# Kernel optimization log

Hardware: AMD Instinct MI355X
Metric: run time of the kernel (lower is better)

## Reference

```python
import jax, jax.numpy as jnp
import numpy as np

B, N, A = 2, 4096, 5
TOPK = 30
K_RBF = 16
MAX_AA = 22
MAXREL = 32
EDGE_IN = 16 + K_RBF * 25 + 14 + 16  # 446
EDGE_FEAT = 128
PI = 3.1415926


def l2norm(v, eps=1e-12):
    n = jnp.sqrt(jnp.sum(v * v, axis=-1, keepdims=True))
    return v / jnp.maximum(n, eps)


def gather_nodes(nodes, idx):
    # nodes: (B,N,C), idx: (B,N,K) -> (B,N,K,C)
    b, n, k = idx.shape
    flat = idx.reshape(b, n * k, 1)
    out = jnp.take_along_axis(nodes, flat, axis=1)
    return out.reshape(b, n, k, nodes.shape[-1])


def quaternions(R):
    # R: (...,3,3) -> unit quaternion (...,4)
    Rxx, Ryy, Rzz = R[..., 0, 0], R[..., 1, 1], R[..., 2, 2]
    mag = 0.5 * jnp.sqrt(jnp.abs(1.0 + jnp.stack([Rxx - Ryy - Rzz, -Rxx + Ryy - Rzz, -Rxx - Ryy + Rzz], -1)) + 1e-12)
    signs = jnp.sign(jnp.stack([R[..., 2, 1] - R[..., 1, 2], R[..., 0, 2] - R[..., 2, 0], R[..., 1, 0] - R[..., 0, 1]], -1))
    xyz = signs * mag
    w = jnp.sqrt(jax.nn.relu(1.0 + Rxx + Ryy + Rzz) + 1e-12)[..., None] / 2.0
    return l2norm(jnp.concatenate([xyz, w], -1))


def setup_inputs():
    key = jax.random.key(0)
    ks = jax.random.split(key, 12)
    X = jax.random.normal(ks[0], (B, N, A, 3), jnp.float32) * 3.0
    mask = jnp.ones((B, N), jnp.float32)
    mask_atoms = jnp.ones((B, N, A), jnp.float32)
    means = jax.random.normal(ks[1], (K_RBF,), jnp.float32)
    stds = jax.random.normal(ks[2], (K_RBF,), jnp.float32)
    mul_w = jax.random.normal(ks[3], (A * A,), jnp.float32)
    bias_w = jax.random.normal(ks[4], (A * A,), jnp.float32)
    aa_pair_embed = jax.random.normal(ks[5], (MAX_AA * MAX_AA, K_RBF), jnp.float32) * 0.02
    aa_pair_embed = aa_pair_embed.at[441].set(0.0)  # padding_idx
    relpos_embed = jax.random.normal(ks[6], (2 * MAXREL + 1, 16), jnp.float32) * 0.02
    mask_embed = jax.random.normal(ks[7], (2, 16), jnp.float32) * 0.02
    W1 = jax.random.normal(ks[8], (EDGE_IN, EDGE_IN), jnp.float32) / np.sqrt(EDGE_IN)
    b1 = jnp.zeros((EDGE_IN,), jnp.float32)
    W2 = jax.random.normal(ks[9], (EDGE_IN, EDGE_FEAT), jnp.float32) / np.sqrt(EDGE_IN)
    b2 = jnp.zeros((EDGE_FEAT,), jnp.float32)
    aa = jax.random.randint(ks[10], (B, N), 0, 21, jnp.int32)
    residue_idx = jnp.tile(jnp.arange(N, dtype=jnp.int32)[None, :], (B, 1))
    chain_labels = jax.random.randint(ks[11], (B, N), 0, 2, jnp.int32)
    return dict(X=X, mask=mask, mask_atoms=mask_atoms, means=means, stds=stds, mul_w=mul_w,
                bias_w=bias_w, aa_pair_embed=aa_pair_embed, relpos_embed=relpos_embed,
                mask_embed=mask_embed, W1=W1, b1=b1, W2=W2, b2=b2, aa=aa,
                residue_idx=residue_idx, chain_labels=chain_labels)


def reference(X, mask, mask_atoms, means, stds, mul_w, bias_w, aa_pair_embed, relpos_embed,
              mask_embed, W1, b1, W2, b2, aa, residue_idx, chain_labels):
    Ca = X[:, :, 1]  # (B,N,3) C-alpha
    # ---- _dist: spatial kNN over C-alpha ----
    mask2d = mask[:, :, None] * mask[:, None, :]
    dx = Ca[:, None, :, :] - Ca[:, :, None, :]
    D = mask2d * jnp.sqrt(jnp.sum(dx * dx, -1) + 1e-6)
    D_adj = D + (1.0 - mask2d) * jnp.max(D, -1, keepdims=True)
    _, E_idx = jax.lax.top_k(-D_adj, TOPK)  # smallest distances
    mask_attend = jnp.take_along_axis(mask2d, E_idx, axis=2)  # (B,N,K)
    # ---- orientation features (local frames + quaternions) ----
    ones3 = jnp.ones((B, 1, 3), X.dtype)
    u = l2norm(jnp.concatenate([ones3, Ca[:, 1:] - Ca[:, :-1]], 1))
    b_ = l2norm(jnp.concatenate([u[:, :-1] - u[:, 1:], ones3], 1))
    n_ = l2norm(jnp.concatenate([jnp.cross(u[:, :-1], u[:, 1:]), ones3], 1))
    lf = jnp.stack([b_, n_, jnp.cross(b_, n_)], axis=2)  # (B,N,3,3)
    X_nb = gather_nodes(Ca, E_idx)                       # (B,N,K,3)
    O_nb = gather_nodes(lf.reshape(B, N, 9), E_idx).reshape(B, N, TOPK, 3, 3)
    t = X_nb - Ca[:, :, None, :]
    t = jnp.einsum('bnij,bnkj->bnki', lf, t)
    t = l2norm(t) * mask_attend[..., None]
    r = jnp.einsum('bnji,bnkjl->bnkil', lf, O_nb)  # lf^T @ O_nb
    q = quaternions(r) * mask_attend[..., None]
    O_feat = jnp.concatenate([t, q, 1.0 - 2.0 * jnp.abs(t), 1.0 - 2.0 * jnp.abs(q)], -1)  # (B,N,K,14)
    # ---- positional / chain embeddings ----
    offset = residue_idx[:, :, None] - residue_idx[:, None, :]
    offset_nb = jnp.take_along_axis(offset, E_idx, 2)
    d_chain = (chain_labels[:, :, None] == chain_labels[:, None, :]).astype(jnp.int32)
    E_chains = jnp.take_along_axis(d_chain, E_idx, 2)
    d = jnp.clip(offset_nb + MAXREL, 0, 2 * MAXREL)
    E_pos = relpos_embed[d] + mask_embed[E_chains]  # (B,N,K,16)
    # ---- GaussianLayer: aa-pair embed + atom-pair distance RBF ----
    aa_pair = aa[:, :, None] * MAX_AA + aa[:, None, :]
    aa_nb = jnp.take_along_axis(aa_pair, E_idx, 2)
    feat_aapair = aa_pair_embed[aa_nb] * mask_attend[..., None]  # (B,N,K,16)
    nbX = gather_nodes(X.reshape(B, N, A * 3), E_idx).reshape(B, N, TOPK, A, 3)
    delta = nbX[:, :, :, :, None, :] - X[:, :, None, None, :, :]  # (B,N,K,A,A,3)
    Dab = jnp.sqrt(jnp.sum(delta * delta, -1) + 1e-12)            # (B,N,K,A,A)
    et = jnp.arange(A * A).reshape(A, A)
    xg = mul_w[et] * Dab + bias_w[et]
    m_nb = gather_nodes(mask_atoms, E_idx)  # (B,N,K,A)
    xg = xg * (m_nb[..., None, :] * m_nb[..., :, None])
    std = jnp.abs(stds) + 0.01
    g = jnp.exp(-0.5 * ((xg[..., None] - means) / std) ** 2) / ((2.0 * PI) ** 0.5 * std)
    gbf = g.reshape(B, N, TOPK, A * A * K_RBF) * mask_attend[..., None]  # (B,N,K,400)
    # ---- fuse and project (NonLinear gbf_proj) ----
    E = jnp.concatenate([E_pos, gbf, O_feat, feat_aapair], -1)  # (B,N,K,446)
    h = jax.nn.gelu(E @ W1 + b1, approximate=False)
    return h @ W2 + b2  # (B,N,K,128)
```

## Files before the change

kernel.cpp:

```cpp
#include <hip/hip_runtime.h>
#include <cstdint>
#include <cstddef>

#define NN 4096
#define TOPK_ 30
#define BN_TOT 8192
#define M_TOT 245760
#define KP 448
#define HSTRIDE 136
#define EF 128

typedef unsigned short u16;
typedef unsigned int u32;
typedef __attribute__((ext_vector_type(8))) short bf16x8;
typedef __attribute__((ext_vector_type(4))) float f32x4;

__device__ __forceinline__ float b2f(u16 u){ return __uint_as_float(((u32)u)<<16); }
__device__ __forceinline__ u16 f2b(float f){
  u32 u = __float_as_uint(f);
  return (u16)((u + 0x7FFFu + ((u>>16)&1u)) >> 16);
}
__device__ __forceinline__ float ldf(const void* p, long i, int fl){
  return fl ? ((const float*)p)[i] : b2f(((const u16*)p)[i]);
}
__device__ __forceinline__ int is_f32_flag(const u16* mask){
  return (((const u32*)mask)[0] == 0x3F800000u) ? 1 : 0;
}
__device__ __forceinline__ void norm3(float x,float y,float z,float&ox,float&oy,float&oz){
  float n = sqrtf(x*x+y*y+z*z); n = fmaxf(n, 1e-12f);
  ox=x/n; oy=y/n; oz=z/n;
}
__device__ __forceinline__ float sgn(float x){ return x>0.f?1.f:(x<0.f?-1.f:0.f); }
__device__ __forceinline__ float gelu_fast(float x){
  float y = 0.70710678118654752440f * x;
  float s = fabsf(y);
  float t = __builtin_amdgcn_rcpf(fmaf(0.3275911f, s, 1.0f));
  float p = fmaf(fmaf(fmaf(fmaf(1.061405429f, t, -1.453152027f), t, 1.421413741f), t,
                 -0.284496736f), t, 0.254829592f);
  float e = __expf(-y*y);
  float erfs = fmaf(-p*t, e, 1.0f);
  float erfy = (x >= 0.f) ? erfs : -erfs;
  float hx = 0.5f*x;
  return fmaf(hx, erfy, hx);
}
__device__ __forceinline__ u32 pk_bf16(float lo, float hi){
  u32 r;
  asm("v_cvt_pk_bf16_f32 %0, %1, %2" : "=v"(r) : "v"(lo), "v"(hi));
  return r;
}

__global__ __launch_bounds__(256) void prep_kernel(
    const void* __restrict__ X, const u16* __restrict__ mask,
    const void* __restrict__ W1, const void* __restrict__ b1,
    const void* __restrict__ W2, const void* __restrict__ b2,
    float* __restrict__ ca, float* __restrict__ lf,
    u16* __restrict__ W1P, u16* __restrict__ W2P,
    float* __restrict__ b1p, float* __restrict__ b2p)
{
  const int fl = is_f32_flag(mask);
  int idx = blockIdx.x*256 + threadIdx.x;
  if (idx < BN_TOT) {
    int i = idx & (NN-1);
    float cax = ldf(X, (long)idx*15+3, fl), cay = ldf(X, (long)idx*15+4, fl), caz = ldf(X, (long)idx*15+5, fl);
    ca[idx*4+0]=cax; ca[idx*4+1]=cay; ca[idx*4+2]=caz; ca[idx*4+3]=0.f;
    float bx,by,bz,nx,ny,nz;
    if (i < NN-1) {
      float uix,uiy,uiz;
      if (i==0) { norm3(1.f,1.f,1.f,uix,uiy,uiz); }
      else {
        float px=ldf(X,(long)(idx-1)*15+3,fl), py=ldf(X,(long)(idx-1)*15+4,fl), pz=ldf(X,(long)(idx-1)*15+5,fl);
        norm3(cax-px, cay-py, caz-pz, uix,uiy,uiz);
      }
      float qx=ldf(X,(long)(idx+1)*15+3,fl), qy=ldf(X,(long)(idx+1)*15+4,fl), qz=ldf(X,(long)(idx+1)*15+5,fl);
      float vx,vy,vz; norm3(qx-cax, qy-cay, qz-caz, vx,vy,vz);
      norm3(uix-vx, uiy-vy, uiz-vz, bx,by,bz);
      norm3(uiy*vz-uiz*vy, uiz*vx-uix*vz, uix*vy-uiy*vx, nx,ny,nz);
    } else {
      norm3(1.f,1.f,1.f,bx,by,bz); nx=bx; ny=by; nz=bz;
    }
    float cx = by*nz - bz*ny, cy = bz*nx - bx*nz, cz = bx*ny - by*nx;
    float* L = lf + (size_t)idx*12;
    L[0]=bx;L[1]=by;L[2]=bz;L[3]=nx;L[4]=ny;L[5]=nz;L[6]=cx;L[7]=cy;L[8]=cz;
    return;
  }
  int r1 = idx - BN_TOT;
  if (r1 < 229376) {
    int f = r1 >> 9, li = r1 & 511;
    int n0 = f / 14, kc = f - n0*14;
    int ln = li >> 3, j = li & 7;
    int n = n0*16 + (ln & 15);
    int k = kc*32 + (ln >> 4)*8 + j;
    W1P[r1] = (n < 446 && k < 446) ? (fl ? f2b(((const float*)W1)[(long)k*446 + n])
                                         : ((const u16*)W1)[(long)k*446 + n]) : (u16)0;
    return;
  }
  int r2 = r1 - 229376;
  if (r2 < 65536) {
    int f = r2 >> 9, li = r2 & 511;
    int n0 = f >> 4, kc = f & 15;
    int ln = li >> 3, j = li & 7;
    int n = n0*16 + (ln & 15);
    int k = kc*32 + (ln >> 4)*8 + j;
    W2P[r2] = (k < 446) ? (fl ? f2b(((const float*)W2)[(long)k*128 + n])
                              : ((const u16*)W2)[(long)k*128 + n]) : (u16)0;
    return;
  }
  int r3 = r2 - 65536;
  if (r3 < 512) { b1p[r3] = (r3<446)? ldf(b1, r3, fl) : 0.f; return; }
  int r4 = r3 - 512;
  if (r4 < 128) { b2p[r4] = ldf(b2, r4, fl); }
}

__global__ __launch_bounds__(64) void knn_kernel(const float4* __restrict__ ca,
                                                 int* __restrict__ eidx)
{
#pragma clang fp contract(off)
  __shared__ u32 keys[NN];
  int bi = blockIdx.x;
  int lane = threadIdx.x;
  int b = bi >> 12;
  const float4 ci = ca[bi];
  const float4* cab = ca + (b<<12);
  u32 mind = 0xFFFFFFFFu; int minj = 1<<30;
  for (int c = 0; c < 64; ++c) {
    int j = (c<<6) | lane;
    float4 cj = cab[j];
    float dx = cj.x-ci.x, dy = cj.y-ci.y, dz = cj.z-ci.z;
    float ss = dx*dx;
    ss = ss + dy*dy;
    ss = ss + dz*dz;
    float d = sqrtf(ss + 1e-6f);
    u32 db = __float_as_uint(d);
    keys[(c<<6)|lane] = db;
    if (db < mind) { mind = db; minj = j; }
  }
  __syncthreads();
  for (int r = 0; r < TOPK_; ++r) {
    u32 wd = mind; int wj = minj;
    #pragma unroll
    for (int off = 32; off; off >>= 1) {
      u32 od = __shfl_xor(wd, off, 64);
      int oj = __shfl_xor(wj, off, 64);
      if (od < wd || (od == wd && oj < wj)) { wd = od; wj = oj; }
    }
    if (lane == 0) eidx[bi*TOPK_ + r] = wj;
    int wl = wj & 63;
    if (lane == wl) keys[wj] = 0xFFFFFFFFu;
    __syncthreads();
    u32 kv = keys[(lane<<6)|wl];
    int kj = (lane<<6)|wl;
    #pragma unroll
    for (int off = 32; off; off >>= 1) {
      u32 od = __shfl_xor(kv, off, 64);
      int oj = __shfl_xor(kj, off, 64);
      if (od < kv || (od == kv && oj < kj)) { kv = od; kj = oj; }
    }
    if (lane == wl) { mind = kv; minj = kj; }
  }
}

__global__ __launch_bounds__(512,2) void mega_mlp(
    const void* __restrict__ X, const u16* __restrict__ mask, const void* __restrict__ mask_atoms,
    const void* __restrict__ means, const void* __restrict__ stds,
    const void* __restrict__ mul_w, const void* __restrict__ bias_w,
    const void* __restrict__ aa_pe, const void* __restrict__ relpos, const void* __restrict__ mask_emb,
    const int* __restrict__ aa, const int* __restrict__ ridx, const int* __restrict__ chains,
    const int* __restrict__ eidx, const float* __restrict__ ca, const float* __restrict__ lf,
    const u16* __restrict__ W1P, const u16* __restrict__ W2P,
    const float* __restrict__ b1p, const float* __restrict__ b2p,
    void* __restrict__ C)
{
  __shared__ __align__(16) u16 Et[128*448];
  __shared__ float Dabs[128][29];
  __shared__ float maA[128];
  const int fl = is_f32_flag(mask);
  int tid = threadIdx.x;
  int lane = tid & 63, wave = tid >> 6;
  int wr = wave >> 2, wc = wave & 3;
  int rowBase = blockIdx.x * 128;

  {
    int eo = tid >> 2, q = tid & 3;
    int e = rowBase + eo;
    int bi = (int)((unsigned)e / 30u);
    int k = e - bi*30;
    int bj = ((bi >> 12) << 12) + eidx[bi*TOPK_ + k];
    if (q == 1) maA[eo] = ldf(mask, bi, fl) * ldf(mask, bj, fl);
    float Xi[15];
    #pragma unroll
    for (int v = 0; v < 15; ++v) Xi[v] = ldf(X, (long)bi*15 + v, fl);
    for (int a = q; a < 5; a += 4) {
      float xj0 = ldf(X,(long)bj*15 + a*3+0, fl);
      float xj1 = ldf(X,(long)bj*15 + a*3+1, fl);
      float xj2 = ldf(X,(long)bj*15 + a*3+2, fl);
      float mja = ldf(mask_atoms,(long)bj*5 + a, fl);
      #pragma unroll
      for (int c = 0; c < 5; ++c) {
        float d0 = xj0 - Xi[c*3+0];
        float d1 = xj1 - Xi[c*3+1];
        float d2 = xj2 - Xi[c*3+2];
        float Dab = sqrtf(d0*d0 + d1*d1 + d2*d2 + 1e-12f);
        float mm = mja * ldf(mask_atoms,(long)bj*5 + c, fl);
        float mw = ldf(mul_w, a*5+c, fl), bw = ldf(bias_w, a*5+c, fl);
        Dabs[eo][a*5+c] = (mw*Dab + bw) * mm;
      }
    }
  }

  if (tid < 128) {
    int eo = tid;
    int e = rowBase + eo;
    int bi = (int)((unsigned)e / 30u);
    int k = e - bi*30;
    int bj = ((bi >> 12) << 12) + eidx[bi*TOPK_ + k];
    float ma = ldf(mask, bi, fl) * ldf(mask, bj, fl);
    char* rowB = (char*)Et + eo*896;
    int xr = (eo & 7) << 4;
    {
      int d = ridx[bi] - ridx[bj] + 32; d = d < 0 ? 0 : (d > 64 ? 64 : d);
      int ch = (chains[bi] == chains[bj]) ? 1 : 0;
      uint4 wA;
      wA.x = pk_bf16(ldf(relpos,d*16+0,fl)+ldf(mask_emb,ch*16+0,fl),
                     ldf(relpos,d*16+1,fl)+ldf(mask_emb,ch*16+1,fl));
      wA.y = pk_bf16(ldf(relpos,d*16+2,fl)+ldf(mask_emb,ch*16+2,fl),
                     ldf(relpos,d*16+3,fl)+ldf(mask_emb,ch*16+3,fl));
      wA.z = pk_bf16(ldf(relpos,d*16+4,fl)+ldf(mask_emb,ch*16+4,fl),
                     ldf(relpos,d*16+5,fl)+ldf(mask_emb,ch*16+5,fl));
      wA.w = pk_bf16(ldf(relpos,d*16+6,fl)+ldf(mask_emb,ch*16+6,fl),
                     ldf(relpos,d*16+7,fl)+ldf(mask_emb,ch*16+7,fl));
      *(uint4*)(rowB + (0 ^ xr)) = wA;
      uint4 wB;
      wB.x = pk_bf16(ldf(relpos,d*16+8,fl)+ldf(mask_emb,ch*16+8,fl),
                     ldf(relpos,d*16+9,fl)+ldf(mask_emb,ch*16+9,fl));
      wB.y = pk_bf16(ldf(relpos,d*16+10,fl)+ldf(mask_emb,ch*16+10,fl),
                     ldf(relpos,d*16+11,fl)+ldf(mask_emb,ch*16+11,fl));
      wB.z = pk_bf16(ldf(relpos,d*16+12,fl)+ldf(mask_emb,ch*16+12,fl),
                     ldf(relpos,d*16+13,fl)+ldf(mask_emb,ch*16+13,fl));
      wB.w = pk_bf16(ldf(relpos,d*16+14,fl)+ldf(mask_emb,ch*16+14,fl),
                     ldf(relpos,d*16+15,fl)+ldf(mask_emb,ch*16+15,fl));
      *(uint4*)(rowB + (16 ^ xr)) = wB;
    }
    float t0,t1,t2,q0,q1,q2,qw;
    {
      float Li[9], Lj[9];
      #pragma unroll
      for (int q_ = 0; q_ < 9; ++q_) { Li[q_] = lf[(size_t)bi*12+q_]; Lj[q_] = lf[(size_t)bj*12+q_]; }
      float dx = ca[bj*4+0]-ca[bi*4+0], dy = ca[bj*4+1]-ca[bi*4+1], dz = ca[bj*4+2]-ca[bi*4+2];
      t0 = Li[0]*dx+Li[1]*dy+Li[2]*dz;
      t1 = Li[3]*dx+Li[4]*dy+Li[5]*dz;
      t2 = Li[6]*dx+Li[7]*dy+Li[8]*dz;
      float tn = fmaxf(sqrtf(t0*t0+t1*t1+t2*t2), 1e-12f);
      t0 = t0/tn*ma; t1 = t1/tn*ma; t2 = t2/tn*ma;
      float R00=Li[0]*Lj[0]+Li[3]*Lj[3]+Li[6]*Lj[6];
      float R01=Li[0]*Lj[1]+Li[3]*Lj[4]+Li[6]*Lj[7];
      float R02=Li[0]*Lj[2]+Li[3]*Lj[5]+Li[6]*Lj[8];
      float R10=Li[1]*Lj[0]+Li[4]*Lj[3]+Li[7]*Lj[6];
      float R11=Li[1]*Lj[1]+Li[4]*Lj[4]+Li[7]*Lj[7];
      float R12=Li[1]*Lj[2]+Li[4]*Lj[5]+Li[7]*Lj[8];
      float R20=Li[2]*Lj[0]+Li[5]*Lj[3]+Li[8]*Lj[6];
      float R21=Li[2]*Lj[1]+Li[5]*Lj[4]+Li[8]*Lj[7];
      float R22=Li[2]*Lj[2]+Li[5]*Lj[5]+Li[8]*Lj[8];
      float m0 = 0.5f*sqrtf(fabsf(1.f+R00-R11-R22)+1e-12f);
      float m1 = 0.5f*sqrtf(fabsf(1.f-R00+R11-R22)+1e-12f);
      float m2 = 0.5f*sqrtf(fabsf(1.f-R00-R11+R22)+1e-12f);
      q0 = sgn(R21-R12)*m0; q1 = sgn(R02-R20)*m1; q2 = sgn(R10-R01)*m2;
      qw = 0.5f*sqrtf(fmaxf(1.f+R00+R11+R22, 0.f)+1e-12f);
      float qn = fmaxf(sqrtf(q0*q0+q1*q1+q2*q2+qw*qw), 1e-12f);
      q0 = q0/qn*ma; q1 = q1/qn*ma; q2 = q2/qn*ma; qw = qw/qn*ma;
    }
    int aap = aa[bi]*22 + aa[bj];
    {
      uint4 w0;
      w0.x = pk_bf16(t0, t1);  w0.y = pk_bf16(t2, q0);
      w0.z = pk_bf16(q1, q2);  w0.w = pk_bf16(qw, 1.f-2.f*fabsf(t0));
      *(uint4*)(rowB + (832 ^ xr)) = w0;
    }
    {
      uint4 w1;
      w1.x = pk_bf16(1.f-2.f*fabsf(t1), 1.f-2.f*fabsf(t2));
      w1.y = pk_bf16(1.f-2.f*fabsf(q0), 1.f-2.f*fabsf(q1));
      w1.z = pk_bf16(1.f-2.f*fabsf(q2), 1.f-2.f*fabsf(qw));
      w1.w = pk_bf16(ldf(aa_pe, aap*16+0, fl)*ma, ldf(aa_pe, aap*16+1, fl)*ma);
      *(uint4*)(rowB + (848 ^ xr)) = w1;
    }
    {
      uint4 w2;
      w2.x = pk_bf16(ldf(aa_pe, aap*16+2, fl)*ma, ldf(aa_pe, aap*16+3, fl)*ma);
      w2.y = pk_bf16(ldf(aa_pe, aap*16+4, fl)*ma, ldf(aa_pe, aap*16+5, fl)*ma);
      w2.z = pk_bf16(ldf(aa_pe, aap*16+6, fl)*ma, ldf(aa_pe, aap*16+7, fl)*ma);
      w2.w = pk_bf16(ldf(aa_pe, aap*16+8, fl)*ma, ldf(aa_pe, aap*16+9, fl)*ma);
      *(uint4*)(rowB + (864 ^ xr)) = w2;
    }
    {
      uint4 w3;
      w3.x = pk_bf16(ldf(aa_pe, aap*16+10, fl)*ma, ldf(aa_pe, aap*16+11, fl)*ma);
      w3.y = pk_bf16(ldf(aa_pe, aap*16+12, fl)*ma, ldf(aa_pe, aap*16+13, fl)*ma);
      w3.z = pk_bf16(ldf(aa_pe, aap*16+14, fl)*ma, ldf(aa_pe, aap*16+15, fl)*ma);
      w3.w = 0u;
      *(uint4*)(rowB + (880 ^ xr)) = w3;
    }
  }
  __syncthreads();

  {
    float meanv[16], rinvv[16], coefv[16];
    #pragma unroll
    for (int r = 0; r < 16; ++r) {
      meanv[r] = ldf(means, r, fl);
      float sd = fabsf(ldf(stds, r, fl)) + 0.01f;
      rinvv[r] = 1.0f / sd;
      coefv[r] = 0.3989422804014327f * rinvv[r];
    }
    #pragma unroll 1
    for (int i = 0; i < 13; ++i) {
      int G = tid + i*512;
      if (G < 6400) {
        int row = (int)((unsigned)G / 50u);
        int gp = G - row*50;
        float xg = Dabs[row][gp >> 1];
        float ma = maA[row];
        int odd = gp & 1;
        u32 w[4];
        #pragma unroll
        for (int j2 = 0; j2 < 4; ++j2) {
          float me0 = odd ? meanv[j2*2+8]   : meanv[j2*2];
          float ri0 = odd ? rinvv[j2*2+8]   : rinvv[j2*2];
          float co0 = odd ? coefv[j2*2+8]   : coefv[j2*2];
          float me1 = odd ? meanv[j2*2+9]   : meanv[j2*2+1];
          float ri1 = odd ? rinvv[j2*2+9]   : rinvv[j2*2+1];
          float co1 = odd ? coefv[j2*2+9]   : coefv[j2*2+1];
          float z0 = (xg - me0) * ri0;
          float z1 = (xg - me1) * ri1;
          float v0 = __expf(-0.5f*z0*z0) * co0 * ma;
          float v1 = __expf(-0.5f*z1*z1) * co1 * ma;
          w[j2] = pk_bf16(v0, v1);
        }
        uint4 W4; W4.x = w[0]; W4.y = w[1]; W4.z = w[2]; W4.w = w[3];
        *(uint4*)((char*)Et + row*896 + ((32 + (gp<<4)) ^ ((row&7)<<4))) = W4;
      }
    }
  }
  __syncthreads();

  f32x4 acc1[4][4][2] = {};
  #pragma unroll 1
  for (int t = 0; t < 7; ++t) {
    bf16x8 af[2][4];
    #pragma unroll
    for (int kk = 0; kk < 2; ++kk)
      #pragma unroll
      for (int r = 0; r < 4; ++r) {
        int row = wr*64 + r*16 + (lane&15);
        int s = kk*4 + (lane>>4);
        af[kk][r] = *(const bf16x8*)(Et + row*448 + t*64 + ((s ^ (row&7))<<3));
      }
    bf16x8 bgA[2][2][2];
    #pragma unroll
    for (int c = 0; c < 2; ++c)
      #pragma unroll
      for (int cc = 0; cc < 2; ++cc)
        #pragma unroll
        for (int kk = 0; kk < 2; ++kk)
          bgA[c][cc][kk] = *(const bf16x8*)(W1P + (((c*8 + wc*2 + cc)*14 + t*2 + kk) << 9) + lane*8);
    #pragma unroll
    for (int c = 0; c < 2; ++c)
      #pragma unroll
      for (int r = 0; r < 4; ++r)
        #pragma unroll
        for (int cc = 0; cc < 2; ++cc)
          #pragma unroll
          for (int kk = 0; kk < 2; ++kk)
            acc1[c][r][cc] = __builtin_amdgcn_mfma_f32_16x16x32_bf16(af[kk][r], bgA[c][cc][kk], acc1[c][r][cc], 0,0,0);
    bf16x8 bgB[2][2][2];
    #pragma unroll
    for (int c = 0; c < 2; ++c)
      #pragma unroll
      for (int cc = 0; cc < 2; ++cc)
        #pragma unroll
        for (int kk = 0; kk < 2; ++kk)
          bgB[c][cc][kk] = *(const bf16x8*)(W1P + ((((c+2)*8 + wc*2 + cc)*14 + t*2 + kk) << 9) + lane*8);
    #pragma unroll
    for (int c = 0; c < 2; ++c)
      #pragma unroll
      for (int r = 0; r < 4; ++r)
        #pragma unroll
        for (int cc = 0; cc < 2; ++cc)
          #pragma unroll
          for (int kk = 0; kk < 2; ++kk)
            acc1[c+2][r][cc] = __builtin_amdgcn_mfma_f32_16x16x32_bf16(af[kk][r], bgB[c][cc][kk], acc1[c+2][r][cc], 0,0,0);
  }

  u16* hs0 = Et;
  u16* hs1 = Et + 128*HSTRIDE;
  #define STORE_HS(cN, buf) do {                                                  \
    _Pragma("unroll")                                                             \
    for (int r = 0; r < 4; ++r) {                                                 \
      _Pragma("unroll")                                                           \
      for (int cc = 0; cc < 2; ++cc) {                                            \
        int col = wc*32 + cc*16 + (lane & 15);                                    \
        float bv = b1p[(cN)*128 + col];                                           \
        int row0 = wr*64 + r*16 + (lane>>4)*4;                                    \
        u32 p01 = pk_bf16(gelu_fast(acc1[cN][r][cc][0]+bv),                       \
                          gelu_fast(acc1[cN][r][cc][1]+bv));                      \
        u32 p23 = pk_bf16(gelu_fast(acc1[cN][r][cc][2]+bv),                       \
                          gelu_fast(acc1[cN][r][cc][3]+bv));                      \
        u16* hb_ = (buf) + row0*HSTRIDE + col;                                    \
        hb_[0]         = (u16)p01; hb_[HSTRIDE]   = (u16)(p01>>16);               \
        hb_[2*HSTRIDE] = (u16)p23; hb_[3*HSTRIDE] = (u16)(p23>>16);               \
      }                                                                           \
    }                                                                             \
  } while(0)

  f32x4 acc2[4][2] = {};
  __syncthreads();
  STORE_HS(0, hs0);
  __syncthreads();
  #pragma unroll
  for (int c = 0; c < 4; ++c) {
    u16* hb = (c & 1) ? hs1 : hs0;
    u16* hn = (c & 1) ? hs0 : hs1;
    if (c < 3) STORE_HS(c+1, hn);
    #pragma unroll
    for (int k2 = 0; k2 < 4; ++k2) {
      bf16x8 af2[4], bg2[2];
      #pragma unroll
      for (int r = 0; r < 4; ++r) {
        int row = wr*64 + r*16 + (lane&15);
        af2[r] = *(const bf16x8*)(hb + row*HSTRIDE + k2*32 + (lane>>4)*8);
      }
      #pragma unroll
      for (int cc = 0; cc < 2; ++cc)
        bg2[cc] = *(const bf16x8*)(W2P + ((((wc*2+cc)*16) + c*4 + k2) << 9) + lane*8);
      #pragma unroll
      for (int r = 0; r < 4; ++r)
        #pragma unroll
        for (int cc = 0; cc < 2; ++cc)
          acc2[r][cc] = __builtin_amdgcn_mfma_f32_16x16x32_bf16(af2[r], bg2[cc], acc2[r][cc], 0,0,0);
    }
    __syncthreads();
  }
  #undef STORE_HS

  const int f32out = is_f32_flag(mask);
  #pragma unroll
  for (int r = 0; r < 4; ++r) {
    #pragma unroll
    for (int cc = 0; cc < 2; ++cc) {
      int col = wc*32 + cc*16 + (lane & 15);
      float bv = b2p[col];
      #pragma unroll
      for (int g = 0; g < 4; ++g) {
        long row = (long)rowBase + wr*64 + r*16 + (lane>>4)*4 + g;
        float v = acc2[r][cc][g] + bv;
        long o = row*EF + col;
        if (f32out) ((float*)C)[o] = v;
        else        ((u16*)C)[o]  = f2b(v);
      }
    }
  }
}

extern "C" void kernel_launch(void* const* d_in, const int* in_sizes, int n_in,
                              void* d_out, int out_size, void* d_ws, size_t ws_size,
                              hipStream_t stream) {
  const void* X          = d_in[0];
  const u16* mask        = (const u16*)d_in[1];
  const void* mask_atoms = d_in[2];
  const void* means      = d_in[3];
  const void* stds       = d_in[4];
  const void* mul_w      = d_in[5];
  const void* bias_w     = d_in[6];
  const void* aa_pe      = d_in[7];
  const void* relpos     = d_in[8];
  const void* mask_emb   = d_in[9];
  const void* W1         = d_in[10];
  const void* b1         = d_in[11];
  const void* W2         = d_in[12];
  const void* b2         = d_in[13];
  const int* aa          = (const int*)d_in[14];
  const int* ridx        = (const int*)d_in[15];
  const int* chains      = (const int*)d_in[16];

  char* ws = (char*)d_ws;
  float* ca  = (float*)(ws + 0);
  float* lf  = (float*)(ws + 131072);
  int* eidx  = (int*)(ws + 524288);
  u16* W1P   = (u16*)(ws + 1507328);
  u16* W2P   = (u16*)(ws + 1966080);
  float* b1p = (float*)(ws + 2097152);
  float* b2p = (float*)(ws + 2099200);

  prep_kernel<<<1187, 256, 0, stream>>>(X, mask, W1, b1, W2, b2, ca, lf, W1P, W2P, b1p, b2p);
  knn_kernel<<<BN_TOT, 64, 0, stream>>>((const float4*)ca, eidx);
  mega_mlp<<<M_TOT/128, 512, 0, stream>>>(X, mask, mask_atoms, means, stds, mul_w, bias_w,
                                          aa_pe, relpos, mask_emb, aa, ridx, chains,
                                          eidx, ca, lf, W1P, W2P, b1p, b2p, d_out);
}
```

Before: 728.8 us.

## Pack per-residue inputs and RBF constants in prep, vectorize gathers, hoist GELU

```diff
diff --git a/kernel.cpp b/kernel.cpp
--- a/kernel.cpp
+++ b/kernel.cpp
@@ -48,21 +48,62 @@
   asm("v_cvt_pk_bf16_f32 %0, %1, %2" : "=v"(r) : "v"(lo), "v"(hi));
   return r;
 }
+__device__ __forceinline__ void ld16(const void* p, int row, int fl, float* o){
+  if (fl) {
+    const float4* q = (const float4*)((const float*)p + (long)row*16);
+    float4 a=q[0], b=q[1], c=q[2], d=q[3];
+    o[0]=a.x; o[1]=a.y; o[2]=a.z; o[3]=a.w;
+    o[4]=b.x; o[5]=b.y; o[6]=b.z; o[7]=b.w;
+    o[8]=c.x; o[9]=c.y; o[10]=c.z; o[11]=c.w;
+    o[12]=d.x; o[13]=d.y; o[14]=d.z; o[15]=d.w;
+  } else {
+    const uint4* q = (const uint4*)((const u16*)p + (long)row*16);
+    uint4 a=q[0], b=q[1];
+    o[0]=__uint_as_float(a.x<<16);  o[1]=__uint_as_float(a.x&0xFFFF0000u);
+    o[2]=__uint_as_float(a.y<<16);  o[3]=__uint_as_float(a.y&0xFFFF0000u);
+    o[4]=__uint_as_float(a.z<<16);  o[5]=__uint_as_float(a.z&0xFFFF0000u);
+    o[6]=__uint_as_float(a.w<<16);  o[7]=__uint_as_float(a.w&0xFFFF0000u);
+    o[8]=__uint_as_float(b.x<<16);  o[9]=__uint_as_float(b.x&0xFFFF0000u);
+    o[10]=__uint_as_float(b.y<<16); o[11]=__uint_as_float(b.y&0xFFFF0000u);
+    o[12]=__uint_as_float(b.z<<16); o[13]=__uint_as_float(b.z&0xFFFF0000u);
+    o[14]=__uint_as_float(b.w<<16); o[15]=__uint_as_float(b.w&0xFFFF0000u);
+  }
+}
 
 __global__ __launch_bounds__(256) void prep_kernel(
     const void* __restrict__ X, const u16* __restrict__ mask,
+    const void* __restrict__ mask_atoms,
+    const void* __restrict__ means, const void* __restrict__ stds,
+    const void* __restrict__ mul_w, const void* __restrict__ bias_w,
     const void* __restrict__ W1, const void* __restrict__ b1,
     const void* __restrict__ W2, const void* __restrict__ b2,
     float* __restrict__ ca, float* __restrict__ lf,
     u16* __restrict__ W1P, u16* __restrict__ W2P,
-    float* __restrict__ b1p, float* __restrict__ b2p)
+    float* __restrict__ b1p, float* __restrict__ b2p,
+    float* __restrict__ Fp, float* __restrict__ wsc)
 {
   const int fl = is_f32_flag(mask);
   int idx = blockIdx.x*256 + threadIdx.x;
   if (idx < BN_TOT) {
     int i = idx & (NN-1);
-    float cax = ldf(X, (long)idx*15+3, fl), cay = ldf(X, (long)idx*15+4, fl), caz = ldf(X, (long)idx*15+5, fl);
+    float xr[15];
+    #pragma unroll
+    for (int v = 0; v < 15; ++v) xr[v] = ldf(X, (long)idx*15+v, fl);
+    float cax = xr[3], cay = xr[4], caz = xr[5];
     ca[idx*4+0]=cax; ca[idx*4+1]=cay; ca[idx*4+2]=caz; ca[idx*4+3]=0.f;
+    {
+      float mres = ldf(mask, idx, fl);
+      float m0 = ldf(mask_atoms,(long)idx*5+0,fl), m1 = ldf(mask_atoms,(long)idx*5+1,fl);
+      float m2 = ldf(mask_atoms,(long)idx*5+2,fl), m3 = ldf(mask_atoms,(long)idx*5+3,fl);
+      float m4 = ldf(mask_atoms,(long)idx*5+4,fl);
+      float4* F4 = (float4*)(Fp + (long)idx*24);
+      F4[0] = make_float4(xr[0],xr[1],xr[2],xr[3]);
+      F4[1] = make_float4(xr[4],xr[5],xr[6],xr[7]);
+      F4[2] = make_float4(xr[8],xr[9],xr[10],xr[11]);
+      F4[3] = make_float4(xr[12],xr[13],xr[14],mres);
+      F4[4] = make_float4(m0,m1,m2,m3);
+      F4[5] = make_float4(m4,0.f,0.f,0.f);
+    }
     float bx,by,bz,nx,ny,nz;
     if (i < NN-1) {
       float uix,uiy,uiz;
@@ -108,7 +149,18 @@
   int r3 = r2 - 65536;
   if (r3 < 512) { b1p[r3] = (r3<446)? ldf(b1, r3, fl) : 0.f; return; }
   int r4 = r3 - 512;
-  if (r4 < 128) { b2p[r4] = ldf(b2, r4, fl); }
+  if (r4 < 128) { b2p[r4] = ldf(b2, r4, fl); return; }
+  int r5 = r4 - 128;
+  if (r5 < 16) {
+    float sd = fabsf(ldf(stds, r5, fl)) + 0.01f;
+    float ri = 1.0f / sd;
+    wsc[r5] = ldf(means, r5, fl);
+    wsc[16 + r5] = ri;
+    wsc[32 + r5] = 0.3989422804014327f * ri;
+    return;
+  }
+  if (r5 < 41) { wsc[48 + (r5-16)] = ldf(mul_w, r5-16, fl); return; }
+  if (r5 < 66) { wsc[73 + (r5-41)] = ldf(bias_w, r5-41, fl); }
 }
 
 __global__ __launch_bounds__(64) void knn_kernel(const float4* __restrict__ ca,
@@ -160,9 +212,8 @@
 }
 
 __global__ __launch_bounds__(512,2) void mega_mlp(
-    const void* __restrict__ X, const u16* __restrict__ mask, const void* __restrict__ mask_atoms,
-    const void* __restrict__ means, const void* __restrict__ stds,
-    const void* __restrict__ mul_w, const void* __restrict__ bias_w,
+    const float* __restrict__ Fp, const float* __restrict__ wsc,
+    const u16* __restrict__ mask,
     const void* __restrict__ aa_pe, const void* __restrict__ relpos, const void* __restrict__ mask_emb,
     const int* __restrict__ aa, const int* __restrict__ ridx, const int* __restrict__ chains,
     const int* __restrict__ eidx, const float* __restrict__ ca, const float* __restrict__ lf,
@@ -185,24 +236,33 @@
     int bi = (int)((unsigned)e / 30u);
     int k = e - bi*30;
     int bj = ((bi >> 12) << 12) + eidx[bi*TOPK_ + k];
-    if (q == 1) maA[eo] = ldf(mask, bi, fl) * ldf(mask, bj, fl);
+    const float* Fi = Fp + (long)bi*24;
+    const float* Fj = Fp + (long)bj*24;
     float Xi[15];
-    #pragma unroll
-    for (int v = 0; v < 15; ++v) Xi[v] = ldf(X, (long)bi*15 + v, fl);
+    {
+      const float4* F4 = (const float4*)Fi;
+      float4 A=F4[0], B=F4[1], Cc=F4[2], D=F4[3];
+      Xi[0]=A.x;Xi[1]=A.y;Xi[2]=A.z;Xi[3]=A.w;
+      Xi[4]=B.x;Xi[5]=B.y;Xi[6]=B.z;Xi[7]=B.w;
+      Xi[8]=Cc.x;Xi[9]=Cc.y;Xi[10]=Cc.z;Xi[11]=Cc.w;
+      Xi[12]=D.x;Xi[13]=D.y;Xi[14]=D.z;
+      if (q == 1) maA[eo] = D.w * Fj[15];
+    }
+    float4 Mj = *(const float4*)(Fj + 16);
+    float  Mj4 = Fj[20];
     for (int a = q; a < 5; a += 4) {
-      float xj0 = ldf(X,(long)bj*15 + a*3+0, fl);
-      float xj1 = ldf(X,(long)bj*15 + a*3+1, fl);
-      float xj2 = ldf(X,(long)bj*15 + a*3+2, fl);
-      float mja = ldf(mask_atoms,(long)bj*5 + a, fl);
+      float xj0 = Fj[a*3+0], xj1 = Fj[a*3+1], xj2 = Fj[a*3+2];
+      float mja = (a==0)?Mj.x:(a==1)?Mj.y:(a==2)?Mj.z:(a==3)?Mj.w:Mj4;
+      mja = Fj[16+a];
       #pragma unroll
       for (int c = 0; c < 5; ++c) {
         float d0 = xj0 - Xi[c*3+0];
         float d1 = xj1 - Xi[c*3+1];
         float d2 = xj2 - Xi[c*3+2];
         float Dab = sqrtf(d0*d0 + d1*d1 + d2*d2 + 1e-12f);
-        float mm = mja * ldf(mask_atoms,(long)bj*5 + c, fl);
-        float mw = ldf(mul_w, a*5+c, fl), bw = ldf(bias_w, a*5+c, fl);
-        Dabs[eo][a*5+c] = (mw*Dab + bw) * mm;
+        float mjc = (c==0)?Mj.x:(c==1)?Mj.y:(c==2)?Mj.z:(c==3)?Mj.w:Mj4;
+        float mw = wsc[48 + a*5+c], bw = wsc[73 + a*5+c];
+        Dabs[eo][a*5+c] = (mw*Dab + bw) * (mja * mjc);
       }
     }
   }
@@ -213,39 +273,41 @@
     int bi = (int)((unsigned)e / 30u);
     int k = e - bi*30;
     int bj = ((bi >> 12) << 12) + eidx[bi*TOPK_ + k];
-    float ma = ldf(mask, bi, fl) * ldf(mask, bj, fl);
+    float ma = Fp[(long)bi*24+15] * Fp[(long)bj*24+15];
     char* rowB = (char*)Et + eo*896;
     int xr = (eo & 7) << 4;
     {
       int d = ridx[bi] - ridx[bj] + 32; d = d < 0 ? 0 : (d > 64 ? 64 : d);
       int ch = (chains[bi] == chains[bj]) ? 1 : 0;
-      uint4 wA;
-      wA.x = pk_bf16(ldf(relpos,d*16+0,fl)+ldf(mask_emb,ch*16+0,fl),
-                     ldf(relpos,d*16+1,fl)+ldf(mask_emb,ch*16+1,fl));
-      wA.y = pk_bf16(ldf(relpos,d*16+2,fl)+ldf(mask_emb,ch*16+2,fl),
-                     ldf(relpos,d*16+3,fl)+ldf(mask_emb,ch*16+3,fl));
-      wA.z = pk_bf16(ldf(relpos,d*16+4,fl)+ldf(mask_emb,ch*16+4,fl),
-                     ldf(relpos,d*16+5,fl)+ldf(mask_emb,ch*16+5,fl));
-      wA.w = pk_bf16(ldf(relpos,d*16+6,fl)+ldf(mask_emb,ch*16+6,fl),
-                     ldf(relpos,d*16+7,fl)+ldf(mask_emb,ch*16+7,fl));
-      *(uint4*)(rowB + (0 ^ xr)) = wA;
-      uint4 wB;
-      wB.x = pk_bf16(ldf(relpos,d*16+8,fl)+ldf(mask_emb,ch*16+8,fl),
-                     ldf(relpos,d*16+9,fl)+ldf(mask_emb,ch*16+9,fl));
-      wB.y = pk_bf16(ldf(relpos,d*16+10,fl)+ldf(mask_emb,ch*16+10,fl),
-                     ldf(relpos,d*16+11,fl)+ldf(mask_emb,ch*16+11,fl));
-      wB.z = pk_bf16(ldf(relpos,d*16+12,fl)+ldf(mask_emb,ch*16+12,fl),
-                     ldf(relpos,d*16+13,fl)+ldf(mask_emb,ch*16+13,fl));
-      wB.w = pk_bf16(ldf(relpos,d*16+14,fl)+ldf(mask_emb,ch*16+14,fl),
-                     ldf(relpos,d*16+15,fl)+ldf(mask_emb,ch*16+15,fl));
+      float rp[16], me[16];
+      ld16(relpos, d, fl, rp);
+      ld16(mask_emb, ch, fl, me);
+      uint4 wA, wB;
+      wA.x = pk_bf16(rp[0]+me[0],  rp[1]+me[1]);
+      wA.y = pk_bf16(rp[2]+me[2],  rp[3]+me[3]);
+      wA.z = pk_bf16(rp[4]+me[4],  rp[5]+me[5]);
+      wA.w = pk_bf16(rp[6]+me[6],  rp[7]+me[7]);
+      wB.x = pk_bf16(rp[8]+me[8],  rp[9]+me[9]);
+      wB.y = pk_bf16(rp[10]+me[10],rp[11]+me[11]);
+      wB.z = pk_bf16(rp[12]+me[12],rp[13]+me[13]);
+      wB.w = pk_bf16(rp[14]+me[14],rp[15]+me[15]);
+      *(uint4*)(rowB + (0 ^ xr))  = wA;
       *(uint4*)(rowB + (16 ^ xr)) = wB;
     }
     float t0,t1,t2,q0,q1,q2,qw;
     {
       float Li[9], Lj[9];
-      #pragma unroll
-      for (int q_ = 0; q_ < 9; ++q_) { Li[q_] = lf[(size_t)bi*12+q_]; Lj[q_] = lf[(size_t)bj*12+q_]; }
-      float dx = ca[bj*4+0]-ca[bi*4+0], dy = ca[bj*4+1]-ca[bi*4+1], dz = ca[bj*4+2]-ca[bi*4+2];
+      {
+        const float4* L4 = (const float4*)(lf + (size_t)bi*12);
+        float4 a=L4[0], b=L4[1], c=L4[2];
+        Li[0]=a.x;Li[1]=a.y;Li[2]=a.z;Li[3]=a.w;Li[4]=b.x;Li[5]=b.y;Li[6]=b.z;Li[7]=b.w;Li[8]=c.x;
+        const float4* M4 = (const float4*)(lf + (size_t)bj*12);
+        float4 d=M4[0], e2=M4[1], f=M4[2];
+        Lj[0]=d.x;Lj[1]=d.y;Lj[2]=d.z;Lj[3]=d.w;Lj[4]=e2.x;Lj[5]=e2.y;Lj[6]=e2.z;Lj[7]=e2.w;Lj[8]=f.x;
+      }
+      float4 ci = *(const float4*)(ca + bj*4);
+      float4 c0 = *(const float4*)(ca + bi*4);
+      float dx = ci.x-c0.x, dy = ci.y-c0.y, dz = ci.z-c0.z;
       t0 = Li[0]*dx+Li[1]*dy+Li[2]*dz;
       t1 = Li[3]*dx+Li[4]*dy+Li[5]*dz;
       t2 = Li[6]*dx+Li[7]*dy+Li[8]*dz;
@@ -268,35 +330,24 @@
       float qn = fmaxf(sqrtf(q0*q0+q1*q1+q2*q2+qw*qw), 1e-12f);
       q0 = q0/qn*ma; q1 = q1/qn*ma; q2 = q2/qn*ma; qw = qw/qn*ma;
     }
-    int aap = aa[bi]*22 + aa[bj];
     {
-      uint4 w0;
+      int aap = aa[bi]*22 + aa[bj];
+      float av[16];
+      ld16(aa_pe, aap, fl, av);
+      uint4 w0, w1, w2, w3;
       w0.x = pk_bf16(t0, t1);  w0.y = pk_bf16(t2, q0);
       w0.z = pk_bf16(q1, q2);  w0.w = pk_bf16(qw, 1.f-2.f*fabsf(t0));
-      *(uint4*)(rowB + (832 ^ xr)) = w0;
-    }
-    {
-      uint4 w1;
       w1.x = pk_bf16(1.f-2.f*fabsf(t1), 1.f-2.f*fabsf(t2));
       w1.y = pk_bf16(1.f-2.f*fabsf(q0), 1.f-2.f*fabsf(q1));
       w1.z = pk_bf16(1.f-2.f*fabsf(q2), 1.f-2.f*fabsf(qw));
-      w1.w = pk_bf16(ldf(aa_pe, aap*16+0, fl)*ma, ldf(aa_pe, aap*16+1, fl)*ma);
+      w1.w = pk_bf16(av[0]*ma, av[1]*ma);
+      w2.x = pk_bf16(av[2]*ma, av[3]*ma);   w2.y = pk_bf16(av[4]*ma, av[5]*ma);
+      w2.z = pk_bf16(av[6]*ma, av[7]*ma);   w2.w = pk_bf16(av[8]*ma, av[9]*ma);
+      w3.x = pk_bf16(av[10]*ma, av[11]*ma); w3.y = pk_bf16(av[12]*ma, av[13]*ma);
+      w3.z = pk_bf16(av[14]*ma, av[15]*ma); w3.w = 0u;
+      *(uint4*)(rowB + (832 ^ xr)) = w0;
       *(uint4*)(rowB + (848 ^ xr)) = w1;
-    }
-    {
-      uint4 w2;
-      w2.x = pk_bf16(ldf(aa_pe, aap*16+2, fl)*ma, ldf(aa_pe, aap*16+3, fl)*ma);
-      w2.y = pk_bf16(ldf(aa_pe, aap*16+4, fl)*ma, ldf(aa_pe, aap*16+5, fl)*ma);
-      w2.z = pk_bf16(ldf(aa_pe, aap*16+6, fl)*ma, ldf(aa_pe, aap*16+7, fl)*ma);
-      w2.w = pk_bf16(ldf(aa_pe, aap*16+8, fl)*ma, ldf(aa_pe, aap*16+9, fl)*ma);
       *(uint4*)(rowB + (864 ^ xr)) = w2;
-    }
-    {
-      uint4 w3;
-      w3.x = pk_bf16(ldf(aa_pe, aap*16+10, fl)*ma, ldf(aa_pe, aap*16+11, fl)*ma);
-      w3.y = pk_bf16(ldf(aa_pe, aap*16+12, fl)*ma, ldf(aa_pe, aap*16+13, fl)*ma);
-      w3.z = pk_bf16(ldf(aa_pe, aap*16+14, fl)*ma, ldf(aa_pe, aap*16+15, fl)*ma);
-      w3.w = 0u;
       *(uint4*)(rowB + (880 ^ xr)) = w3;
     }
   }
@@ -304,12 +355,15 @@
 
   {
     float meanv[16], rinvv[16], coefv[16];
-    #pragma unroll
-    for (int r = 0; r < 16; ++r) {
-      meanv[r] = ldf(means, r, fl);
-      float sd = fabsf(ldf(stds, r, fl)) + 0.01f;
-      rinvv[r] = 1.0f / sd;
-      coefv[r] = 0.3989422804014327f * rinvv[r];
+    {
+      const float4* W4 = (const float4*)wsc;
+      #pragma unroll
+      for (int g = 0; g < 4; ++g) {
+        float4 m = W4[g], r = W4[4+g], c = W4[8+g];
+        meanv[g*4+0]=m.x; meanv[g*4+1]=m.y; meanv[g*4+2]=m.z; meanv[g*4+3]=m.w;
+        rinvv[g*4+0]=r.x; rinvv[g*4+1]=r.y; rinvv[g*4+2]=r.z; rinvv[g*4+3]=r.w;
+        coefv[g*4+0]=c.x; coefv[g*4+1]=c.y; coefv[g*4+2]=c.z; coefv[g*4+3]=c.w;
+      }
     }
     #pragma unroll 1
     for (int i = 0; i < 13; ++i) {
@@ -323,20 +377,20 @@
         u32 w[4];
         #pragma unroll
         for (int j2 = 0; j2 < 4; ++j2) {
-          float me0 = odd ? meanv[j2*2+8]   : meanv[j2*2];
-          float ri0 = odd ? rinvv[j2*2+8]   : rinvv[j2*2];
-          float co0 = odd ? coefv[j2*2+8]   : coefv[j2*2];
-          float me1 = odd ? meanv[j2*2+9]   : meanv[j2*2+1];
-          float ri1 = odd ? rinvv[j2*2+9]   : rinvv[j2*2+1];
-          float co1 = odd ? coefv[j2*2+9]   : coefv[j2*2+1];
+          float me0 = odd ? meanv[j2*2+8] : meanv[j2*2];
+          float ri0 = odd ? rinvv[j2*2+8] : rinvv[j2*2];
+          float co0 = odd ? coefv[j2*2+8] : coefv[j2*2];
+          float me1 = odd ? meanv[j2*2+9] : meanv[j2*2+1];
+          float ri1 = odd ? rinvv[j2*2+9] : rinvv[j2*2+1];
+          float co1 = odd ? coefv[j2*2+9] : coefv[j2*2+1];
           float z0 = (xg - me0) * ri0;
           float z1 = (xg - me1) * ri1;
           float v0 = __expf(-0.5f*z0*z0) * co0 * ma;
           float v1 = __expf(-0.5f*z1*z1) * co1 * ma;
           w[j2] = pk_bf16(v0, v1);
         }
-        uint4 W4; W4.x = w[0]; W4.y = w[1]; W4.z = w[2]; W4.w = w[3];
-        *(uint4*)((char*)Et + row*896 + ((32 + (gp<<4)) ^ ((row&7)<<4))) = W4;
+        uint4 W4o; W4o.x = w[0]; W4o.y = w[1]; W4o.z = w[2]; W4o.w = w[3];
+        *(uint4*)((char*)Et + row*896 + ((32 + (gp<<4)) ^ ((row&7)<<4))) = W4o;
       }
     }
   }
@@ -389,6 +443,21 @@
           for (int kk = 0; kk < 2; ++kk)
             acc1[c+2][r][cc] = __builtin_amdgcn_mfma_f32_16x16x32_bf16(af[kk][r], bgB[c][cc][kk], acc1[c+2][r][cc], 0,0,0);
   }
+
+  u32 hpk[4][4][2][2];
+  #pragma unroll
+  for (int c = 0; c < 4; ++c)
+    #pragma unroll
+    for (int r = 0; r < 4; ++r)
+      #pragma unroll
+      for (int cc = 0; cc < 2; ++cc) {
+        int col = wc*32 + cc*16 + (lane & 15);
+        float bv = b1p[c*128 + col];
+        hpk[c][r][cc][0] = pk_bf16(gelu_fast(acc1[c][r][cc][0]+bv),
+                                   gelu_fast(acc1[c][r][cc][1]+bv));
+        hpk[c][r][cc][1] = pk_bf16(gelu_fast(acc1[c][r][cc][2]+bv),
+                                   gelu_fast(acc1[c][r][cc][3]+bv));
+      }
 
   u16* hs0 = Et;
   u16* hs1 = Et + 128*HSTRIDE;
@@ -398,12 +467,8 @@
       _Pragma("unroll")                                                           \
       for (int cc = 0; cc < 2; ++cc) {                                            \
         int col = wc*32 + cc*16 + (lane & 15);                                    \
-        float bv = b1p[(cN)*128 + col];                                           \
         int row0 = wr*64 + r*16 + (lane>>4)*4;                                    \
-        u32 p01 = pk_bf16(gelu_fast(acc1[cN][r][cc][0]+bv),                       \
-                          gelu_fast(acc1[cN][r][cc][1]+bv));                      \
-        u32 p23 = pk_bf16(gelu_fast(acc1[cN][r][cc][2]+bv),                       \
-                          gelu_fast(acc1[cN][r][cc][3]+bv));                      \
+        u32 p01 = hpk[cN][r][cc][0], p23 = hpk[cN][r][cc][1];                     \
         u16* hb_ = (buf) + row0*HSTRIDE + col;                                    \
         hb_[0]         = (u16)p01; hb_[HSTRIDE]   = (u16)(p01>>16);               \
         hb_[2*HSTRIDE] = (u16)p23; hb_[3*HSTRIDE] = (u16)(p23>>16);               \
@@ -441,7 +506,7 @@
   }
   #undef STORE_HS
 
-  const int f32out = is_f32_flag(mask);
+  const int f32out = fl;
   #pragma unroll
   for (int r = 0; r < 4; ++r) {
     #pragma unroll
@@ -489,10 +554,13 @@
   u16* W2P   = (u16*)(ws + 1966080);
   float* b1p = (float*)(ws + 2097152);
   float* b2p = (float*)(ws + 2099200);
-
-  prep_kernel<<<1187, 256, 0, stream>>>(X, mask, W1, b1, W2, b2, ca, lf, W1P, W2P, b1p, b2p);
+  float* wsc = (float*)(ws + 2099712);
+  float* Fp  = (float*)(ws + 2100224);
+
+  prep_kernel<<<1187, 256, 0, stream>>>(X, mask, mask_atoms, means, stds, mul_w, bias_w,
+                                        W1, b1, W2, b2, ca, lf, W1P, W2P, b1p, b2p, Fp, wsc);
   knn_kernel<<<BN_TOT, 64, 0, stream>>>((const float4*)ca, eidx);
-  mega_mlp<<<M_TOT/128, 512, 0, stream>>>(X, mask, mask_atoms, means, stds, mul_w, bias_w,
+  mega_mlp<<<M_TOT/128, 512, 0, stream>>>(Fp, wsc, mask,
                                           aa_pe, relpos, mask_emb, aa, ridx, chains,
                                           eidx, ca, lf, W1P, W2P, b1p, b2p, d_out);
 }
```

Result: faster. 709.3 us (-2.7%).
